# Kernel optimization log

Measured on AMD Instinct MI355X. Metric: run time of the kernel, lower is better.

Reference implementation:

```python
import jax, jax.numpy as jnp
import numpy as np

N_NODES = 20000
N_EDGES = 640000
CHANNELS = 128
EDGE_ATTR_DIM = 1


def setup_inputs() -> dict:
    key = jax.random.key(0)
    ks = jax.random.split(key, 10)
    C, E, N = CHANNELS, N_EDGES, N_NODES
    x_a = jax.random.normal(ks[0], (N, C), dtype=jnp.float32)
    edge_index = jax.random.randint(ks[1], (2, E), 0, N, dtype=jnp.int64)
    edge_attr = jax.random.uniform(ks[2], (E, EDGE_ATTR_DIM), dtype=jnp.float32)
    # Linear params (stored as [in, out]); scaled like torch default init
    g_in = 2 * C + EDGE_ATTR_DIM
    g_w = jax.random.uniform(ks[3], (g_in, C), jnp.float32, -1, 1) / np.sqrt(g_in)
    g_b = jax.random.uniform(ks[4], (C,), jnp.float32, -1, 1) / np.sqrt(g_in)
    f_w = jax.random.uniform(ks[5], (2 * C, C), jnp.float32, -1, 1) / np.sqrt(2 * C)
    f_b = jax.random.uniform(ks[6], (C,), jnp.float32, -1, 1) / np.sqrt(2 * C)
    cls_w = jax.random.uniform(ks[7], (C, 1), jnp.float32, -1, 1) / np.sqrt(C)
    cls_b = jax.random.uniform(ks[8], (1,), jnp.float32, -1, 1) / np.sqrt(C)
    return {"x_a": x_a, "edge_index": edge_index, "edge_attr": edge_attr,
            "g_w": g_w, "g_b": g_b, "f_w": f_w, "f_b": f_b,
            "cls_w": cls_w, "cls_b": cls_b}


def reference(x_a, edge_index, edge_attr, g_w, g_b, f_w, f_b, cls_w, cls_b):
    # PyG MessagePassing (flow source_to_target): x_j = x[src], x_i = x[dst]
    src = edge_index[0]
    dst = edge_index[1]
    N = x_a.shape[0]
    # message: g([x_i, x_j, e_ij])  -> [E, C]
    z_ij = jnp.concatenate([x_a[dst], x_a[src], edge_attr], axis=-1)
    msg = z_ij @ g_w + g_b
    # aggregate: scatter-mean over destination nodes (empty nodes -> 0)
    sums = jax.ops.segment_sum(msg, dst, num_segments=N)
    cnt = jax.ops.segment_sum(jnp.ones((dst.shape[0], 1), x_a.dtype), dst,
                              num_segments=N)
    aggr = sums / jnp.maximum(cnt, 1.0)
    # update: f([x, aggr])
    h = jnp.concatenate([x_a, aggr], axis=-1) @ f_w + f_b
    # classifier + sigmoid + threshold
    probs = jax.nn.sigmoid(h @ cls_w + cls_b)
    y = probs > 0.5
    return (y, probs)
```

## Files before the change

### kernel.cpp

```cpp
#include <hip/hip_runtime.h>
#include <math.h>

#define NNODES 20000
#define NEDGES 640000
#define C 128

#define NB 64
#define BT 1024

#define CNT_SHIFT 26
#define EDGE_BIAS (1 << 19)
#define SUM_MASK 0x03FFFFFFu

__global__ void __launch_bounds__(1024)
k_weights(const float* __restrict__ g_w, const float* __restrict__ g_b,
          const float* __restrict__ f_w, const float* __restrict__ f_b,
          const float* __restrict__ cls_w, const float* __restrict__ cls_b,
          float* __restrict__ u, float* __restrict__ p,
          float* __restrict__ q, float* __restrict__ scal)
{
    __shared__ float csh[C], vsh[C], red[1024];
    int t    = threadIdx.x;
    int pair = t >> 2;
    int prt  = t & 3;
    int k = pair & 127;
    int h = pair >> 7;

    if (t < C) csh[t] = cls_w[t];
    __syncthreads();

    const float4* fw4 = (const float4*)f_w;
    const float4* gw4 = (const float4*)g_w;
    const float4* cs4 = (const float4*)csh;

    {
        const float4* row = fw4 + (size_t)(h * C + k) * (C / 4) + prt * 8;
        const float4* cc  = cs4 + prt * 8;
        float s = 0.f;
        #pragma unroll
        for (int j = 0; j < 8; ++j) {
            float4 a = row[j], c = cc[j];
            s += a.x * c.x + a.y * c.y + a.z * c.z + a.w * c.w;
        }
        red[t] = s;
    }
    __syncthreads();
    if (prt == 0) {
        float tot = red[t] + red[t + 1] + red[t + 2] + red[t + 3];
        if (h == 0) u[k] = tot;
        else        vsh[k] = tot;
    }
    __syncthreads();

    const float4* vs4 = (const float4*)vsh;
    {
        const float4* row = gw4 + (size_t)(h * C + k) * (C / 4) + prt * 8;
        const float4* vv  = vs4 + prt * 8;
        float s = 0.f;
        #pragma unroll
        for (int j = 0; j < 8; ++j) {
            float4 a = row[j], c = vv[j];
            s += a.x * c.x + a.y * c.y + a.z * c.z + a.w * c.w;
        }
        red[t] = s;
    }
    __syncthreads();
    if (prt == 0) {
        float tot = red[t] + red[t + 1] + red[t + 2] + red[t + 3];
        if (h == 0) p[k] = tot;
        else        q[k] = tot;
    }
    __syncthreads();

    if (t < C) red[t] = g_b[t] * vsh[t];
    __syncthreads();
    for (int s = 64; s > 0; s >>= 1) { if (t < s) red[t] += red[t + s]; __syncthreads(); }
    if (t == 0) scal[0] = red[0];
    __syncthreads();
    if (t < C) red[t] = g_w[256 * C + t] * vsh[t];
    __syncthreads();
    for (int s = 64; s > 0; s >>= 1) { if (t < s) red[t] += red[t + s]; __syncthreads(); }
    if (t == 0) scal[1] = red[0];
    __syncthreads();
    if (t < C) red[t] = f_b[t] * csh[t];
    __syncthreads();
    for (int s = 64; s > 0; s >>= 1) { if (t < s) red[t] += red[t + s]; __syncthreads(); }
    if (t == 0) scal[2] = red[0] + cls_b[0];
}

__global__ void k_node(const float* __restrict__ x,
                       const float* __restrict__ u, const float* __restrict__ p,
                       const float* __restrict__ q,
                       float* __restrict__ xu, float* __restrict__ xp,
                       float* __restrict__ r)
{
    int gtid = blockIdx.x * blockDim.x + threadIdx.x;
    int node = gtid >> 6;
    int lane = threadIdx.x & 63;
    if (node >= NNODES) return;

    const float2* x2 = (const float2*)(x + (size_t)node * C);
    float2 xx = x2[lane];
    float2 uu = ((const float2*)u)[lane];
    float2 pp = ((const float2*)p)[lane];
    float2 qq = ((const float2*)q)[lane];

    float du = xx.x * uu.x + xx.y * uu.y;
    float dp = xx.x * pp.x + xx.y * pp.y;
    float dq = xx.x * qq.x + xx.y * qq.y;

    for (int off = 32; off > 0; off >>= 1) {
        du += __shfl_down(du, off);
        dp += __shfl_down(dp, off);
        dq += __shfl_down(dq, off);
    }
    if (lane == 0) {
        xu[node] = du;
        xp[node] = dp;
        r[node]  = dq;
    }
}

__global__ void __launch_bounds__(BT)
k_edge(const int* __restrict__ ei, const float* __restrict__ attr,
       const float* __restrict__ r, const float* __restrict__ scal,
       unsigned int* __restrict__ part)
{
    __shared__ unsigned int lacc[NNODES];
    int tid = threadIdx.x;

    uint4* l4 = (uint4*)lacc;
    for (int i = tid; i < NNODES / 4; i += BT) l4[i] = make_uint4(0u, 0u, 0u, 0u);
    __syncthreads();

    float gev = scal[1];
    for (int e = blockIdx.x * BT + tid; e < NEDGES; e += NB * BT) {
        int s = ei[e];
        int d = ei[NEDGES + e];
        float t = r[s] + attr[e] * gev;
        int fix = __float2int_rn(t * 65536.0f);
        atomicAdd(&lacc[d], (1u << CNT_SHIFT) + (unsigned int)(fix + EDGE_BIAS));
    }
    __syncthreads();

    uint4* mp4 = (uint4*)(part + (size_t)blockIdx.x * NNODES);
    for (int i = tid; i < NNODES / 4; i += BT) mp4[i] = l4[i];
}

__global__ void k_final(const float* __restrict__ xu, const float* __restrict__ xp,
                        const unsigned int* __restrict__ part,
                        const float* __restrict__ scal, float* __restrict__ out)
{
    int d = blockIdx.x * blockDim.x + threadIdx.x;
    if (d >= NNODES) return;

    int sumfix = 0, cnt = 0;
    #pragma unroll 8
    for (int b = 0; b < NB; ++b) {
        unsigned int v = part[(size_t)b * NNODES + d];
        int c = (int)(v >> CNT_SHIFT);
        cnt += c;
        sumfix += (int)(v & SUM_MASK) - (c << 19);
    }

    float sacc = (float)sumfix * (1.0f / 65536.0f);
    float cmax = fmaxf((float)cnt, 1.0f);
    float cfac = (cnt > 0) ? 1.0f : 0.0f;
    float logit = xu[d] + cfac * (xp[d] + scal[0]) + sacc / cmax + scal[2];
    float pr = 1.0f / (1.0f + expf(-logit));
    out[d] = (pr > 0.5f) ? 1.0f : 0.0f;
    out[NNODES + d] = pr;
}

extern "C" void kernel_launch(void* const* d_in, const int* in_sizes, int n_in,
                              void* d_out, int out_size, void* d_ws, size_t ws_size,
                              hipStream_t stream) {
    const float* x_a       = (const float*)d_in[0];
    const int*   ei        = (const int*)d_in[1];
    const float* edge_attr = (const float*)d_in[2];
    const float* g_w       = (const float*)d_in[3];
    const float* g_b       = (const float*)d_in[4];
    const float* f_w       = (const float*)d_in[5];
    const float* f_b       = (const float*)d_in[6];
    const float* cls_w     = (const float*)d_in[7];
    const float* cls_b     = (const float*)d_in[8];
    float* out = (float*)d_out;

    float* ws   = (float*)d_ws;
    float* u    = ws;
    float* p    = ws + 128;
    float* q    = ws + 256;
    float* scal = ws + 384;
    float* xu   = ws + 512;
    float* xp   = xu + NNODES;
    float* r    = xp + NNODES;
    unsigned int* part = (unsigned int*)(r + NNODES);

    k_weights<<<1, 1024, 0, stream>>>(g_w, g_b, f_w, f_b, cls_w, cls_b, u, p, q, scal);

    k_node<<<(NNODES + 3) / 4, 256, 0, stream>>>(x_a, u, p, q, xu, xp, r);

    k_edge<<<NB, BT, 0, stream>>>(ei, edge_attr, r, scal, part);

    k_final<<<(NNODES + 255) / 256, 256, 0, stream>>>(xu, xp, part, scal, out);
}
```

Measured before the change: 109.5 us.

## Fuse all four kernels into one cooperative kernel with grid syncs

Replaces the four separate launches (weight folding, node projections, edge scatter, final reduction) with a single cooperative kernel that uses grid-wide syncs between phases. Every block recomputes the folded weight vectors redundantly in shared memory, and each thread prefetches its edge indices and attributes into registers before the weight phase so those loads overlap with it. The intent is to remove launch overhead and inter-kernel gaps. In exchange it adds two grid barriers and duplicated weight work in every block, and runs the node projection on only 64 blocks.

```diff
diff --git a/kernel.cpp b/kernel.cpp
--- a/kernel.cpp
+++ b/kernel.cpp
@@ -1,5 +1,8 @@
 #include <hip/hip_runtime.h>
+#include <hip/hip_cooperative_groups.h>
 #include <math.h>
+
+namespace cg = cooperative_groups;
 
 #define NNODES 20000
 #define NEDGES 640000
@@ -7,169 +10,178 @@
 
 #define NB 64
 #define BT 1024
+#define EPT 10
 
 #define CNT_SHIFT 26
 #define EDGE_BIAS (1 << 19)
 #define SUM_MASK 0x03FFFFFFu
 
-__global__ void __launch_bounds__(1024)
-k_weights(const float* __restrict__ g_w, const float* __restrict__ g_b,
-          const float* __restrict__ f_w, const float* __restrict__ f_b,
-          const float* __restrict__ cls_w, const float* __restrict__ cls_b,
-          float* __restrict__ u, float* __restrict__ p,
-          float* __restrict__ q, float* __restrict__ scal)
-{
-    __shared__ float csh[C], vsh[C], red[1024];
-    int t    = threadIdx.x;
-    int pair = t >> 2;
-    int prt  = t & 3;
-    int k = pair & 127;
-    int h = pair >> 7;
-
-    if (t < C) csh[t] = cls_w[t];
-    __syncthreads();
-
-    const float4* fw4 = (const float4*)f_w;
-    const float4* gw4 = (const float4*)g_w;
-    const float4* cs4 = (const float4*)csh;
-
-    {
-        const float4* row = fw4 + (size_t)(h * C + k) * (C / 4) + prt * 8;
-        const float4* cc  = cs4 + prt * 8;
-        float s = 0.f;
-        #pragma unroll
-        for (int j = 0; j < 8; ++j) {
-            float4 a = row[j], c = cc[j];
-            s += a.x * c.x + a.y * c.y + a.z * c.z + a.w * c.w;
-        }
-        red[t] = s;
-    }
-    __syncthreads();
-    if (prt == 0) {
-        float tot = red[t] + red[t + 1] + red[t + 2] + red[t + 3];
-        if (h == 0) u[k] = tot;
-        else        vsh[k] = tot;
-    }
-    __syncthreads();
-
-    const float4* vs4 = (const float4*)vsh;
-    {
-        const float4* row = gw4 + (size_t)(h * C + k) * (C / 4) + prt * 8;
-        const float4* vv  = vs4 + prt * 8;
-        float s = 0.f;
-        #pragma unroll
-        for (int j = 0; j < 8; ++j) {
-            float4 a = row[j], c = vv[j];
-            s += a.x * c.x + a.y * c.y + a.z * c.z + a.w * c.w;
-        }
-        red[t] = s;
-    }
-    __syncthreads();
-    if (prt == 0) {
-        float tot = red[t] + red[t + 1] + red[t + 2] + red[t + 3];
-        if (h == 0) p[k] = tot;
-        else        q[k] = tot;
-    }
-    __syncthreads();
-
-    if (t < C) red[t] = g_b[t] * vsh[t];
-    __syncthreads();
-    for (int s = 64; s > 0; s >>= 1) { if (t < s) red[t] += red[t + s]; __syncthreads(); }
-    if (t == 0) scal[0] = red[0];
-    __syncthreads();
-    if (t < C) red[t] = g_w[256 * C + t] * vsh[t];
-    __syncthreads();
-    for (int s = 64; s > 0; s >>= 1) { if (t < s) red[t] += red[t + s]; __syncthreads(); }
-    if (t == 0) scal[1] = red[0];
-    __syncthreads();
-    if (t < C) red[t] = f_b[t] * csh[t];
-    __syncthreads();
-    for (int s = 64; s > 0; s >>= 1) { if (t < s) red[t] += red[t + s]; __syncthreads(); }
-    if (t == 0) scal[2] = red[0] + cls_b[0];
-}
-
-__global__ void k_node(const float* __restrict__ x,
-                       const float* __restrict__ u, const float* __restrict__ p,
-                       const float* __restrict__ q,
-                       float* __restrict__ xu, float* __restrict__ xp,
-                       float* __restrict__ r)
-{
-    int gtid = blockIdx.x * blockDim.x + threadIdx.x;
-    int node = gtid >> 6;
-    int lane = threadIdx.x & 63;
-    if (node >= NNODES) return;
-
-    const float2* x2 = (const float2*)(x + (size_t)node * C);
-    float2 xx = x2[lane];
-    float2 uu = ((const float2*)u)[lane];
-    float2 pp = ((const float2*)p)[lane];
-    float2 qq = ((const float2*)q)[lane];
-
-    float du = xx.x * uu.x + xx.y * uu.y;
-    float dp = xx.x * pp.x + xx.y * pp.y;
-    float dq = xx.x * qq.x + xx.y * qq.y;
-
-    for (int off = 32; off > 0; off >>= 1) {
-        du += __shfl_down(du, off);
-        dp += __shfl_down(dp, off);
-        dq += __shfl_down(dq, off);
-    }
-    if (lane == 0) {
-        xu[node] = du;
-        xp[node] = dp;
-        r[node]  = dq;
-    }
-}
-
 __global__ void __launch_bounds__(BT)
-k_edge(const int* __restrict__ ei, const float* __restrict__ attr,
-       const float* __restrict__ r, const float* __restrict__ scal,
-       unsigned int* __restrict__ part)
+k_all(const float* __restrict__ x,
+      const int* __restrict__ ei, const float* __restrict__ attr,
+      const float* __restrict__ g_w, const float* __restrict__ g_b,
+      const float* __restrict__ f_w, const float* __restrict__ f_b,
+      const float* __restrict__ cls_w, const float* __restrict__ cls_b,
+      float* __restrict__ xu, float* __restrict__ xp, float* __restrict__ r,
+      unsigned int* __restrict__ part, float* __restrict__ out)
 {
     __shared__ unsigned int lacc[NNODES];
-    int tid = threadIdx.x;
+    __shared__ float csh[C], vsh[C], ush[C], psh[C], qsh[C];
+    __shared__ float red[BT];
+    __shared__ float sgbv, sgev, sc0;
+
+    cg::grid_group grid = cg::this_grid();
+    const int tid  = threadIdx.x;
+    const int gtid = blockIdx.x * BT + tid;
+
+    int   esrc[EPT];
+    int   edst[EPT];
+    float eatt[EPT];
+    #pragma unroll
+    for (int i = 0; i < EPT; ++i) {
+        int e = gtid + i * (NB * BT);
+        bool ok = (e < NEDGES);
+        esrc[i] = ok ? ei[e] : 0;
+        edst[i] = ok ? ei[NEDGES + e] : -1;
+        eatt[i] = ok ? attr[e] : 0.f;
+    }
+
+    {
+        int pair = tid >> 2;
+        int prt  = tid & 3;
+        int k = pair & 127;
+        int h = pair >> 7;
+
+        if (tid < C) csh[tid] = cls_w[tid];
+        __syncthreads();
+
+        const float4* fw4 = (const float4*)f_w;
+        const float4* gw4 = (const float4*)g_w;
+        const float4* cs4 = (const float4*)csh;
+
+        {
+            const float4* row = fw4 + (size_t)(h * C + k) * (C / 4) + prt * 8;
+            const float4* cc  = cs4 + prt * 8;
+            float s = 0.f;
+            #pragma unroll
+            for (int j = 0; j < 8; ++j) {
+                float4 a = row[j], c = cc[j];
+                s += a.x * c.x + a.y * c.y + a.z * c.z + a.w * c.w;
+            }
+            red[tid] = s;
+        }
+        __syncthreads();
+        if (prt == 0) {
+            float tot = red[tid] + red[tid + 1] + red[tid + 2] + red[tid + 3];
+            if (h == 0) ush[k] = tot; else vsh[k] = tot;
+        }
+        __syncthreads();
+
+        const float4* vs4 = (const float4*)vsh;
+        {
+            const float4* row = gw4 + (size_t)(h * C + k) * (C / 4) + prt * 8;
+            const float4* vv  = vs4 + prt * 8;
+            float s = 0.f;
+            #pragma unroll
+            for (int j = 0; j < 8; ++j) {
+                float4 a = row[j], c = vv[j];
+                s += a.x * c.x + a.y * c.y + a.z * c.z + a.w * c.w;
+            }
+            red[tid] = s;
+        }
+        __syncthreads();
+        if (prt == 0) {
+            float tot = red[tid] + red[tid + 1] + red[tid + 2] + red[tid + 3];
+            if (h == 0) psh[k] = tot; else qsh[k] = tot;
+        }
+        __syncthreads();
+
+        if (tid < C) red[tid] = g_b[tid] * vsh[tid];
+        __syncthreads();
+        for (int s = 64; s > 0; s >>= 1) { if (tid < s) red[tid] += red[tid + s]; __syncthreads(); }
+        if (tid == 0) sgbv = red[0];
+        __syncthreads();
+        if (tid < C) red[tid] = g_w[256 * C + tid] * vsh[tid];
+        __syncthreads();
+        for (int s = 64; s > 0; s >>= 1) { if (tid < s) red[tid] += red[tid + s]; __syncthreads(); }
+        if (tid == 0) sgev = red[0];
+        __syncthreads();
+        if (tid < C) red[tid] = f_b[tid] * csh[tid];
+        __syncthreads();
+        for (int s = 64; s > 0; s >>= 1) { if (tid < s) red[tid] += red[tid + s]; __syncthreads(); }
+        if (tid == 0) sc0 = red[0] + cls_b[0];
+        __syncthreads();
+    }
 
     uint4* l4 = (uint4*)lacc;
     for (int i = tid; i < NNODES / 4; i += BT) l4[i] = make_uint4(0u, 0u, 0u, 0u);
+
+    {
+        int w = tid >> 6, lane = tid & 63;
+        int gwave = blockIdx.x * (BT / 64) + w;
+        float2 uu = ((const float2*)ush)[lane];
+        float2 pp = ((const float2*)psh)[lane];
+        float2 qq = ((const float2*)qsh)[lane];
+
+        for (int n = gwave; n < NNODES; n += NB * (BT / 64)) {
+            float2 xx = ((const float2*)(x + (size_t)n * C))[lane];
+            float du = xx.x * uu.x + xx.y * uu.y;
+            float dp = xx.x * pp.x + xx.y * pp.y;
+            float dq = xx.x * qq.x + xx.y * qq.y;
+            for (int off = 32; off > 0; off >>= 1) {
+                du += __shfl_down(du, off);
+                dp += __shfl_down(dp, off);
+                dq += __shfl_down(dq, off);
+            }
+            if (lane == 0) { xu[n] = du; xp[n] = dp; r[n] = dq; }
+        }
+    }
+
+    __threadfence();
+    grid.sync();
+
+    {
+        float gev = sgev;
+        #pragma unroll
+        for (int i = 0; i < EPT; ++i) {
+            int d = edst[i];
+            if (d >= 0) {
+                float t = r[esrc[i]] + eatt[i] * gev;
+                int fix = __float2int_rn(t * 65536.0f);
+                atomicAdd(&lacc[d], (1u << CNT_SHIFT) + (unsigned int)(fix + EDGE_BIAS));
+            }
+        }
+    }
     __syncthreads();
 
-    float gev = scal[1];
-    for (int e = blockIdx.x * BT + tid; e < NEDGES; e += NB * BT) {
-        int s = ei[e];
-        int d = ei[NEDGES + e];
-        float t = r[s] + attr[e] * gev;
-        int fix = __float2int_rn(t * 65536.0f);
-        atomicAdd(&lacc[d], (1u << CNT_SHIFT) + (unsigned int)(fix + EDGE_BIAS));
-    }
-    __syncthreads();
-
-    uint4* mp4 = (uint4*)(part + (size_t)blockIdx.x * NNODES);
-    for (int i = tid; i < NNODES / 4; i += BT) mp4[i] = l4[i];
-}
-
-__global__ void k_final(const float* __restrict__ xu, const float* __restrict__ xp,
-                        const unsigned int* __restrict__ part,
-                        const float* __restrict__ scal, float* __restrict__ out)
-{
-    int d = blockIdx.x * blockDim.x + threadIdx.x;
-    if (d >= NNODES) return;
-
-    int sumfix = 0, cnt = 0;
-    #pragma unroll 8
-    for (int b = 0; b < NB; ++b) {
-        unsigned int v = part[(size_t)b * NNODES + d];
-        int c = (int)(v >> CNT_SHIFT);
-        cnt += c;
-        sumfix += (int)(v & SUM_MASK) - (c << 19);
-    }
-
-    float sacc = (float)sumfix * (1.0f / 65536.0f);
-    float cmax = fmaxf((float)cnt, 1.0f);
-    float cfac = (cnt > 0) ? 1.0f : 0.0f;
-    float logit = xu[d] + cfac * (xp[d] + scal[0]) + sacc / cmax + scal[2];
-    float pr = 1.0f / (1.0f + expf(-logit));
-    out[d] = (pr > 0.5f) ? 1.0f : 0.0f;
-    out[NNODES + d] = pr;
+    {
+        uint4* mp4 = (uint4*)(part + (size_t)blockIdx.x * NNODES);
+        for (int i = tid; i < NNODES / 4; i += BT) mp4[i] = l4[i];
+    }
+
+    __threadfence();
+    grid.sync();
+
+    {
+        int n = blockIdx.x * 313 + tid;
+        if (tid < 313 && n < NNODES) {
+            int sumfix = 0, cnt = 0;
+            #pragma unroll 8
+            for (int b = 0; b < NB; ++b) {
+                unsigned int v = part[(size_t)b * NNODES + n];
+                int c = (int)(v >> CNT_SHIFT);
+                cnt += c;
+                sumfix += (int)(v & SUM_MASK) - (c << 19);
+            }
+            float sacc = (float)sumfix * (1.0f / 65536.0f);
+            float cmax = fmaxf((float)cnt, 1.0f);
+            float cfac = (cnt > 0) ? 1.0f : 0.0f;
+            float logit = xu[n] + cfac * (xp[n] + sgbv) + sacc / cmax + sc0;
+            float pr = 1.0f / (1.0f + expf(-logit));
+            out[n] = (pr > 0.5f) ? 1.0f : 0.0f;
+            out[NNODES + n] = pr;
+        }
+    }
 }
 
 extern "C" void kernel_launch(void* const* d_in, const int* in_sizes, int n_in,
@@ -186,21 +198,17 @@
     const float* cls_b     = (const float*)d_in[8];
     float* out = (float*)d_out;
 
-    float* ws   = (float*)d_ws;
-    float* u    = ws;
-    float* p    = ws + 128;
-    float* q    = ws + 256;
-    float* scal = ws + 384;
-    float* xu   = ws + 512;
-    float* xp   = xu + NNODES;
-    float* r    = xp + NNODES;
-    unsigned int* part = (unsigned int*)(r + NNODES);
-
-    k_weights<<<1, 1024, 0, stream>>>(g_w, g_b, f_w, f_b, cls_w, cls_b, u, p, q, scal);
-
-    k_node<<<(NNODES + 3) / 4, 256, 0, stream>>>(x_a, u, p, q, xu, xp, r);
-
-    k_edge<<<NB, BT, 0, stream>>>(ei, edge_attr, r, scal, part);
-
-    k_final<<<(NNODES + 255) / 256, 256, 0, stream>>>(xu, xp, part, scal, out);
+    unsigned int* part = (unsigned int*)d_ws;
+    float* xu = (float*)d_ws + (size_t)NB * NNODES;
+    float* xp = xu + NNODES;
+    float* r  = xp + NNODES;
+
+    void* args[] = {
+        (void*)&x_a, (void*)&ei, (void*)&edge_attr,
+        (void*)&g_w, (void*)&g_b, (void*)&f_w, (void*)&f_b,
+        (void*)&cls_w, (void*)&cls_b,
+        (void*)&xu, (void*)&xp, (void*)&r, (void*)&part, (void*)&out
+    };
+    hipLaunchCooperativeKernel((const void*)k_all, dim3(NB), dim3(BT),
+                               args, 0, stream);
 }
```

Measured after the change: 201.5 us. 84.0% more time.
